# Kernel tuning notes

Hardware: AMD Instinct MI355X
Metric: run time of the kernel (lower is better)

## Reference

```python
import jax, jax.numpy as jnp
import numpy as np

EPS = 1e-7
INF = 1e8
NUM_CLASSES = 80
SOFT_CENTER_RADIUS = 3.0
TOPK = 13
IOU_WEIGHT = 3.0

B, N, G, C = 16, 8400, 100, NUM_CLASSES
IMG = 640.0


def setup_inputs() -> dict:
    key = jax.random.key(0)
    ks = jax.random.split(key, 8)
    # anchor priors: centers in image, stride column (cx, cy, s, s)
    ctr = jax.random.uniform(ks[0], (N, 2)) * IMG
    stride = jnp.full((N, 1), 8.0)
    priors = jnp.concatenate([ctr, stride, stride], axis=-1)
    # predicted boxes: xyxy around random centers
    pc = jax.random.uniform(ks[1], (B, N, 2)) * IMG
    pwh = jax.random.uniform(ks[2], (B, N, 2)) * 64.0 + 8.0
    pred_bboxes = jnp.concatenate([pc - pwh / 2, pc + pwh / 2], axis=-1)
    pred_scores = jax.random.normal(ks[3], (B, N, C))
    # gt boxes: xyxy
    gc = jax.random.uniform(ks[4], (B, G, 2)) * (IMG - 40.0) + 20.0
    gwh = jax.random.uniform(ks[5], (B, G, 2)) * 128.0 + 16.0
    gt_bboxes = jnp.concatenate([gc - gwh / 2, gc + gwh / 2], axis=-1)
    gt_labels = jax.random.randint(ks[6], (B, G, 1), 0, NUM_CLASSES, dtype=jnp.int32)
    pad_bbox_flag = jnp.ones((B, G, 1), dtype=jnp.float32)
    gt_bboxes_area = gwh[..., 0] * gwh[..., 1]
    area_rule = jnp.array([0.0, 32.0, 96.0, 1.0e4], dtype=jnp.float32)
    return {
        'pred_bboxes': pred_bboxes, 'pred_scores': pred_scores, 'priors': priors,
        'gt_labels': gt_labels, 'gt_bboxes': gt_bboxes, 'pad_bbox_flag': pad_bbox_flag,
        'gt_bboxes_area': gt_bboxes_area, 'area_rule': area_rule,
    }


def _giou(b1, b2):
    # b1, b2 broadcastable [..., 4] xyxy -> GIoU [...]
    lt = jnp.maximum(b1[..., :2], b2[..., :2])
    rb = jnp.minimum(b1[..., 2:], b2[..., 2:])
    wh = jnp.clip(rb - lt, 0.0)
    overlap = wh[..., 0] * wh[..., 1]
    a1 = (b1[..., 2] - b1[..., 0]) * (b1[..., 3] - b1[..., 1])
    a2 = (b2[..., 2] - b2[..., 0]) * (b2[..., 3] - b2[..., 1])
    union = jnp.maximum(a1 + a2 - overlap, EPS)
    iou = overlap / union
    elt = jnp.minimum(b1[..., :2], b2[..., :2])
    erb = jnp.maximum(b1[..., 2:], b2[..., 2:])
    ewh = jnp.clip(erb - elt, 0.0)
    enclose = jnp.maximum(ewh[..., 0] * ewh[..., 1], EPS)
    return iou - (enclose - union) / enclose


def _forward(pred_bboxes, pred_scores, priors, gt_labels, gt_bboxes, pad_bbox_flag,
             gt_bboxes_area, area_rule):
    b, n, _ = pred_bboxes.shape
    g = gt_bboxes.shape[1]
    pts = priors[:, :2]                      # (N,2)
    # point-in-box test -> (B,N,G)
    lt = pts[None, :, None, :] - gt_bboxes[:, None, :, :2]
    rb = gt_bboxes[:, None, :, 2:] - pts[None, :, None, :]
    deltas = jnp.concatenate([lt, rb], axis=-1)          # (B,N,G,4)
    is_in = (jnp.min(deltas, axis=-1) > 0).astype(pred_bboxes.dtype)
    is_in = is_in * pad_bbox_flag[:, None, :, 0]
    # soft center prior
    gt_ctr = (gt_bboxes[..., :2] + gt_bboxes[..., 2:]) / 2.0
    strides = priors[:, 2]
    dist = jnp.sqrt(((pts[None, :, None, :] - gt_ctr[:, None, :, :]) ** 2).sum(-1))
    dist = dist / strides[None, :, None] * is_in
    soft_center_prior = jnp.power(10.0, dist - SOFT_CENTER_RADIUS) * is_in
    # pairwise GIoU (B,N,G)
    giou = _giou(pred_bboxes[:, :, None, :], gt_bboxes[:, None, :, :])
    pairwise_ious = jnp.abs(giou * is_in)
    iou_cost = -jnp.log(pairwise_ious + EPS) * IOU_WEIGHT
    # per-gt-class logit gather: (B,N,G)
    labels = gt_labels[..., 0].astype(jnp.int32)         # (B,G)
    idx = jnp.broadcast_to(labels[:, None, :], (b, n, g))
    logits = jnp.take_along_axis(pred_scores, idx, axis=2)
    sig = jax.nn.sigmoid(logits)
    scale = pairwise_ious - sig
    # stable BCE-with-logits against soft target pairwise_ious
    bce = jnp.maximum(logits, 0.0) - logits * pairwise_ious + jnp.log1p(jnp.exp(-jnp.abs(logits)))
    cls_cost = bce * jnp.exp(jnp.abs(scale) - 1.0) * jnp.abs(scale)
    cost = cls_cost + iou_cost + soft_center_prior
    in_mask = is_in > 0
    cost = jnp.where(in_mask, cost, INF)
    # dynamic-k matching
    k = min(TOPK, n)
    topk_ious = jax.lax.top_k(jnp.transpose(pairwise_ious, (0, 2, 1)), k)[0]  # (B,G,k)
    dyn_k = jnp.clip(topk_ious.sum(-1).astype(jnp.int32), 1, None)            # (B,G)
    ranks = jnp.argsort(jnp.argsort(cost, axis=1), axis=1)                    # (B,N,G)
    valid_gt = pad_bbox_flag[..., 0] > 0                                      # (B,G)
    matching = (ranks < dyn_k[:, None, :]) & valid_gt[:, None, :]             # (B,N,G)
    # resolve anchors matched to >1 gt: keep min-cost gt
    multi = matching.sum(-1) > 1                                              # (B,N)
    onehot_min = jax.nn.one_hot(jnp.argmin(cost, axis=-1), g, dtype=jnp.bool_)
    matching = jnp.where(multi[..., None], onehot_min, matching)
    fg_mask = matching.sum(-1) > 0                                            # (B,N)
    mf = matching.astype(pairwise_ious.dtype)
    matched_ious = (mf * pairwise_ious).sum(-1)                               # (B,N)
    matched_gt = jnp.argmax(mf, axis=-1)                                      # (B,N)
    # dense assignments
    assigned_labels = jnp.where(fg_mask, jnp.take_along_axis(labels, matched_gt, axis=1), NUM_CLASSES)
    gidx = jnp.broadcast_to(matched_gt[..., None], (b, n, 4))
    assigned_bboxes = jnp.where(fg_mask[..., None], jnp.take_along_axis(gt_bboxes, gidx, axis=1), 0.0)
    assign_metrics = jnp.where(fg_mask, matched_ious, 0.0)
    onehot = jax.nn.one_hot(assigned_labels, NUM_CLASSES + 1, dtype=pred_scores.dtype)[..., :NUM_CLASSES]
    assigned_scores = onehot * jnp.where(fg_mask, matched_ious, 1.0)[..., None]
    # per-class positive counts and dynamic class weights
    assigned_labels_num = (onehot * fg_mask[..., None].astype(onehot.dtype)).sum((0, 1))
    maxc = assigned_labels_num.max()
    dynamic_gt_class_weight = jnp.where(assigned_labels_num > 0,
                                        maxc / jnp.maximum(assigned_labels_num, 1.0), 1.0)
    assigned_labels_weights = jnp.where(fg_mask[..., None],
                                        dynamic_gt_class_weight[None, None, :],
                                        jnp.ones((), pred_scores.dtype))
    # gt area distribution (len(area_rule)-1, B, G)
    r2 = area_rule ** 2
    ga = gt_bboxes_area[None]
    area_dist = (ga >= r2[:-1, None, None]) & (ga < r2[1:, None, None]) & valid_gt[None]
    return (assigned_labels.astype(jnp.int32), assigned_labels_weights, assigned_bboxes,
            assigned_scores, assign_metrics, fg_mask, assigned_labels_num,
            dynamic_gt_class_weight, area_dist)


def reference(pred_bboxes, pred_scores, priors, gt_labels, gt_bboxes, pad_bbox_flag,
              gt_bboxes_area, area_rule):
    return _forward(pred_bboxes, pred_scores, priors, gt_labels, gt_bboxes,
                    pad_bbox_flag, gt_bboxes_area, area_rule)
```

## Files before the change

kernel.cpp:

```cpp
#include <hip/hip_runtime.h>

typedef unsigned long long u64;

#define BB 16
#define NN 8400
#define GG 100
#define CC 80
#define KTOP 13
#define EPSF 1e-7f
#define INFC 1e8f
#define MAXIN 1024

static constexpr size_t kO_LAB  = 0;
static constexpr size_t kO_W    = (size_t)BB * NN;
static constexpr size_t kO_BB   = kO_W + (size_t)BB * NN * CC;
static constexpr size_t kO_SC   = kO_BB + (size_t)BB * NN * 4;
static constexpr size_t kO_MET  = kO_SC + (size_t)BB * NN * CC;
static constexpr size_t kO_FG   = kO_MET + (size_t)BB * NN;
static constexpr size_t kO_NUM  = kO_FG + (size_t)BB * NN;
static constexpr size_t kO_DYNW = kO_NUM + CC;
static constexpr size_t kO_AREA = kO_DYNW + CC;

__device__ __forceinline__ unsigned f2u(float x) {
    unsigned b = __float_as_uint(x);
    return (b & 0x80000000u) ? ~b : (b | 0x80000000u);
}
__device__ __forceinline__ float u2f(unsigned e) {
    return __uint_as_float((e & 0x80000000u) ? (e & 0x7fffffffu) : ~e);
}

__device__ __forceinline__ void pair_cost_iou_inside(
    float px, float py, float st,
    float p0, float p1, float p2, float p3,
    float g0, float g1, float g2, float g3,
    float lg, float flag,
    float& cost, float& piou)
{
    float gcx = (g0 + g2) * 0.5f, gcy = (g1 + g3) * 0.5f;
    float dx = px - gcx, dy = py - gcy;
    float dist = sqrtf(dx * dx + dy * dy) / st * flag;
    float scp = exp2f((dist - 3.0f) * 3.32192809488736f) * flag;
    float ix1 = fmaxf(p0, g0), iy1 = fmaxf(p1, g1);
    float ix2 = fminf(p2, g2), iy2 = fminf(p3, g3);
    float ow = fmaxf(ix2 - ix1, 0.0f), oh = fmaxf(iy2 - iy1, 0.0f);
    float ov = ow * oh;
    float a1 = (p2 - p0) * (p3 - p1);
    float a2 = (g2 - g0) * (g3 - g1);
    float uni = fmaxf(a1 + a2 - ov, EPSF);
    float iou = ov / uni;
    float ex1 = fminf(p0, g0), ey1 = fminf(p1, g1);
    float ex2 = fmaxf(p2, g2), ey2 = fmaxf(p3, g3);
    float ew = fmaxf(ex2 - ex1, 0.0f), eh = fmaxf(ey2 - ey1, 0.0f);
    float enc = fmaxf(ew * eh, EPSF);
    float giou = iou - (enc - uni) / enc;
    piou = fabsf(giou * flag);
    float iou_cost = -__logf(piou + EPSF) * 3.0f;
    float sig = 1.0f / (1.0f + __expf(-lg));
    float sc = piou - sig;
    float asc = fabsf(sc);
    float bce = fmaxf(lg, 0.0f) - lg * piou + log1pf(__expf(-fabsf(lg)));
    float cls = bce * __expf(asc - 1.0f) * asc;
    cost = cls + iou_cost + scp;
}

__device__ __forceinline__ void pair_cost_iou(
    float px, float py, float st,
    float p0, float p1, float p2, float p3,
    float g0, float g1, float g2, float g3,
    float lg, float flag,
    float& cost, float& piou)
{
    float l = px - g0, t = py - g1, r = g2 - px, d = g3 - py;
    float mn = fminf(fminf(l, t), fminf(r, d));
    float is_in = (mn > 0.0f) ? flag : 0.0f;
    float gcx = (g0 + g2) * 0.5f, gcy = (g1 + g3) * 0.5f;
    float dx = px - gcx, dy = py - gcy;
    float dist = sqrtf(dx * dx + dy * dy) / st * is_in;
    float scp = exp2f((dist - 3.0f) * 3.32192809488736f) * is_in;
    float ix1 = fmaxf(p0, g0), iy1 = fmaxf(p1, g1);
    float ix2 = fminf(p2, g2), iy2 = fminf(p3, g3);
    float ow = fmaxf(ix2 - ix1, 0.0f), oh = fmaxf(iy2 - iy1, 0.0f);
    float ov = ow * oh;
    float a1 = (p2 - p0) * (p3 - p1);
    float a2 = (g2 - g0) * (g3 - g1);
    float uni = fmaxf(a1 + a2 - ov, EPSF);
    float iou = ov / uni;
    float ex1 = fminf(p0, g0), ey1 = fminf(p1, g1);
    float ex2 = fmaxf(p2, g2), ey2 = fmaxf(p3, g3);
    float ew = fmaxf(ex2 - ex1, 0.0f), eh = fmaxf(ey2 - ey1, 0.0f);
    float enc = fmaxf(ew * eh, EPSF);
    float giou = iou - (enc - uni) / enc;
    piou = fabsf(giou * is_in);
    float iou_cost = -__logf(piou + EPSF) * 3.0f;
    float sig = 1.0f / (1.0f + __expf(-lg));
    float sc = piou - sig;
    float asc = fabsf(sc);
    float bce = fmaxf(lg, 0.0f) - lg * piou + log1pf(__expf(-fabsf(lg)));
    float cls = bce * __expf(asc - 1.0f) * asc;
    float cc = cls + iou_cost + scp;
    cost = (is_in > 0.0f) ? cc : INFC;
}

__global__ __launch_bounds__(256) void k1_match(
    const float* __restrict__ pred_bboxes,
    const float* __restrict__ pred_scores,
    const float* __restrict__ priors,
    const int*   __restrict__ gt_labels,
    const float* __restrict__ gt_bboxes,
    const float* __restrict__ pad_flag,
    int*   __restrict__ match_count,
    int*   __restrict__ match_g,
    float* __restrict__ match_iou)
{
    __shared__ int   s_cnt;
    __shared__ int   s_list[MAXIN];
    __shared__ u64   s_kiou[MAXIN];
    __shared__ u64   s_kcost[MAXIN];
    __shared__ unsigned short s_rc[MAXIN];
    __shared__ float s_top[KTOP];

    int bg = blockIdx.x;
    int b = bg / GG, g = bg - b * GG;
    int tid = threadIdx.x;

    float flag = pad_flag[bg];
    if (flag == 0.0f) return;

    if (tid == 0) s_cnt = 0;
    if (tid < KTOP) s_top[tid] = 0.0f;
    __syncthreads();

    float4 gb = *reinterpret_cast<const float4*>(gt_bboxes + (size_t)bg * 4);

    #pragma unroll 4
    for (int k = 0; k < 32; ++k) {
        int n = tid + (k << 8);
        float4 p = *reinterpret_cast<const float4*>(priors + (size_t)n * 4);
        float mn = fminf(fminf(p.x - gb.x, p.y - gb.y),
                         fminf(gb.z - p.x, gb.w - p.y));
        if (mn > 0.0f) {
            int po = atomicAdd(&s_cnt, 1);
            if (po < MAXIN) s_list[po] = n;
        }
    }
    if (tid < NN - 8192) {
        int n = tid + 8192;
        float4 p = *reinterpret_cast<const float4*>(priors + (size_t)n * 4);
        float mn = fminf(fminf(p.x - gb.x, p.y - gb.y),
                         fminf(gb.z - p.x, gb.w - p.y));
        if (mn > 0.0f) {
            int po = atomicAdd(&s_cnt, 1);
            if (po < MAXIN) s_list[po] = n;
        }
    }
    __syncthreads();
    int M = min(s_cnt, MAXIN);

    if (M == 0) {
        if (tid == 0) {
            int idx = b * NN;
            atomicAdd(&match_count[idx], 1);
            match_g[idx]   = g;
            match_iou[idx] = 0.0f;
        }
        return;
    }

    int lab = gt_labels[bg];

    for (int m = tid; m < M; m += 256) {
        int n = s_list[m];
        float4 pr = *reinterpret_cast<const float4*>(priors + (size_t)n * 4);
        float4 pb = *reinterpret_cast<const float4*>(pred_bboxes + ((size_t)b * NN + n) * 4);
        float lg = pred_scores[((size_t)b * NN + n) * CC + lab];
        float cost, piou;
        pair_cost_iou_inside(pr.x, pr.y, pr.z, pb.x, pb.y, pb.z, pb.w,
                             gb.x, gb.y, gb.z, gb.w, lg, flag, cost, piou);
        s_kiou[m]  = ((u64)f2u(piou) << 32) | (unsigned)n;
        s_kcost[m] = ((u64)f2u(cost) << 32) | (unsigned)n;
    }
    __syncthreads();

    for (int m = tid; m < M; m += 256) {
        u64 ki = s_kiou[m];
        u64 kc = s_kcost[m];
        int riou = 0, rcost = 0;
        #pragma unroll 4
        for (int i = 0; i < M; ++i) {
            riou  += (s_kiou[i]  > ki) ? 1 : 0;
            rcost += (s_kcost[i] < kc) ? 1 : 0;
        }
        if (riou < KTOP) s_top[riou] = u2f((unsigned)(ki >> 32));
        s_rc[m] = (unsigned short)rcost;
    }
    __syncthreads();

    float ksum = 0.0f;
    #pragma unroll
    for (int r = 0; r < KTOP; ++r) ksum += s_top[r];
    int dyn_k = (int)ksum;
    if (dyn_k < 1) dyn_k = 1;

    for (int m = tid; m < M; m += 256) {
        if ((int)s_rc[m] < dyn_k) {
            u64 ki = s_kiou[m];
            int n = (int)(ki & 0xffffffffu);
            int idx = b * NN + n;
            atomicAdd(&match_count[idx], 1);
            match_g[idx]   = g;
            match_iou[idx] = u2f((unsigned)(ki >> 32));
        }
    }
}

__global__ __launch_bounds__(256) void k2_resolve(
    const float* __restrict__ pred_bboxes,
    const float* __restrict__ pred_scores,
    const float* __restrict__ priors,
    const int*   __restrict__ gt_labels,
    const float* __restrict__ gt_bboxes,
    const float* __restrict__ pad_flag,
    const int*   __restrict__ match_count,
    const int*   __restrict__ match_g,
    const float* __restrict__ match_iou,
    int*   __restrict__ r_lab,
    float* __restrict__ r_miou,
    int*   __restrict__ class_num,
    float* __restrict__ out)
{
    int i = blockIdx.x * 256 + threadIdx.x;
    int lane = threadIdx.x & 63;
    int cnt = match_count[i];
    int b = i / NN;

    int lab = CC;
    float miou = 0.0f;
    float4 bbx = make_float4(0.0f, 0.0f, 0.0f, 0.0f);

    if (cnt == 1) {
        int g = match_g[i];
        int gi = b * GG + g;
        miou = match_iou[i];
        lab = gt_labels[gi];
        bbx = *reinterpret_cast<const float4*>(gt_bboxes + (size_t)gi * 4);
    }

    u64 mask = __ballot(cnt > 1);
    while (mask) {
        int src = __builtin_ctzll(mask);
        mask &= mask - 1;
        int ii = (i & ~63) | src;
        int b2 = ii / NN, n2 = ii - b2 * NN;
        float4 pr = *reinterpret_cast<const float4*>(priors + (size_t)n2 * 4);
        float4 pb = *reinterpret_cast<const float4*>(pred_bboxes + (size_t)ii * 4);
        u64 bk = ~0ull; float bp = 0.0f;
        #pragma unroll
        for (int s = 0; s < 2; ++s) {
            int gg = lane + (s << 6);
            if (gg < GG) {
                int gi = b2 * GG + gg;
                float fl = pad_flag[gi];
                float4 gbx = *reinterpret_cast<const float4*>(gt_bboxes + (size_t)gi * 4);
                int lb = gt_labels[gi];
                float lg = pred_scores[(size_t)ii * CC + lb];
                float cost, piou;
                pair_cost_iou(pr.x, pr.y, pr.z, pb.x, pb.y, pb.z, pb.w,
                              gbx.x, gbx.y, gbx.z, gbx.w, lg, fl, cost, piou);
                u64 k = ((u64)f2u(cost) << 32) | (unsigned)gg;
                if (k < bk) { bk = k; bp = piou; }
            }
        }
        #pragma unroll
        for (int off = 1; off < 64; off <<= 1) {
            u64 ok = __shfl_xor(bk, off, 64);
            float op = __shfl_xor(bp, off, 64);
            if (ok < bk) { bk = ok; bp = op; }
        }
        if (lane == src) {
            int gw = (int)(bk & 0xffffffffu);
            int gi = b2 * GG + gw;
            lab = gt_labels[gi];
            miou = bp;
            bbx = *reinterpret_cast<const float4*>(gt_bboxes + (size_t)gi * 4);
        }
    }

    bool fg = cnt > 0;
    if (fg) atomicAdd(&class_num[lab], 1);
    r_lab[i]  = lab;
    r_miou[i] = miou;
    out[kO_LAB + i] = (float)lab;
    out[kO_FG  + i] = fg ? 1.0f : 0.0f;
    out[kO_MET + i] = miou;
    *reinterpret_cast<float4*>(out + kO_BB + (size_t)i * 4) = bbx;
}

#define K4MAIN ((BB * NN * (CC / 4)) / 256)
__global__ __launch_bounds__(256) void k4_fill(
    const int*   __restrict__ r_lab,
    const float* __restrict__ r_miou,
    const int*   __restrict__ class_num,
    const float* __restrict__ gt_area,
    const float* __restrict__ area_rule,
    const float* __restrict__ pad_flag,
    float* __restrict__ out)
{
    __shared__ float s_w[CC];
    int t0 = threadIdx.x;
    if (t0 < 64) {
        int n0 = class_num[t0];
        int n1 = (t0 < CC - 64) ? class_num[t0 + 64] : 0;
        int m = max(n0, n1);
        #pragma unroll
        for (int off = 32; off > 0; off >>= 1) m = max(m, __shfl_down(m, off, 64));
        m = __shfl(m, 0, 64);
        float fm = (float)m;
        s_w[t0] = (n0 > 0) ? fm / fmaxf((float)n0, 1.0f) : 1.0f;
        if (t0 < CC - 64)
            s_w[t0 + 64] = (n1 > 0) ? fm / fmaxf((float)n1, 1.0f) : 1.0f;
    }
    __syncthreads();

    unsigned bid = blockIdx.x;
    if (bid < K4MAIN) {
        unsigned t = bid * 256u + threadIdx.x;
        unsigned i = t / 20u;
        unsigned cq = (t - i * 20u) * 4u;
        int lab = r_lab[i];
        float miou = r_miou[i];
        bool fg = lab < CC;
        unsigned ulab = (unsigned)lab;
        float4 sc, wv;
        sc.x = (ulab == cq + 0u) ? miou : 0.0f;
        sc.y = (ulab == cq + 1u) ? miou : 0.0f;
        sc.z = (ulab == cq + 2u) ? miou : 0.0f;
        sc.w = (ulab == cq + 3u) ? miou : 0.0f;
        wv.x = fg ? s_w[cq + 0u] : 1.0f;
        wv.y = fg ? s_w[cq + 1u] : 1.0f;
        wv.z = fg ? s_w[cq + 2u] : 1.0f;
        wv.w = fg ? s_w[cq + 3u] : 1.0f;
        size_t base = (size_t)i * CC + cq;
        *reinterpret_cast<float4*>(out + kO_SC + base) = sc;
        *reinterpret_cast<float4*>(out + kO_W  + base) = wv;
    } else {
        int idx = (int)(bid - K4MAIN) * 256 + threadIdx.x;
        if (idx < 3 * BB * GG) {
            int z = idx / (BB * GG);
            int rem = idx - z * (BB * GG);
            float ga = gt_area[rem];
            float lo = area_rule[z] * area_rule[z];
            float hi = area_rule[z + 1] * area_rule[z + 1];
            bool v = (ga >= lo) && (ga < hi) && (pad_flag[rem] > 0.0f);
            out[kO_AREA + idx] = v ? 1.0f : 0.0f;
        } else if (idx < 3 * BB * GG + CC) {
            int c = idx - 3 * BB * GG;
            out[kO_NUM + c] = (float)class_num[c];
        } else if (idx < 3 * BB * GG + 2 * CC) {
            int c = idx - 3 * BB * GG - CC;
            out[kO_DYNW + c] = s_w[c];
        }
    }
}

extern "C" void kernel_launch(void* const* d_in, const int* in_sizes, int n_in,
                              void* d_out, int out_size, void* d_ws, size_t ws_size,
                              hipStream_t stream)
{
    const float* pred_bboxes = (const float*)d_in[0];
    const float* pred_scores = (const float*)d_in[1];
    const float* priors      = (const float*)d_in[2];
    const int*   gt_labels   = (const int*)d_in[3];
    const float* gt_bboxes   = (const float*)d_in[4];
    const float* pad_flag    = (const float*)d_in[5];
    const float* gt_area     = (const float*)d_in[6];
    const float* area_rule   = (const float*)d_in[7];
    float* out = (float*)d_out;

    char* w = (char*)d_ws;
    int*   match_count = (int*)w;   w += (size_t)BB * NN * 4;
    int*   class_num   = (int*)w;   w += (size_t)CC * 4;
    int*   match_g     = (int*)w;   w += (size_t)BB * NN * 4;
    float* match_iou   = (float*)w; w += (size_t)BB * NN * 4;
    int*   r_lab       = (int*)w;   w += (size_t)BB * NN * 4;
    float* r_miou      = (float*)w; w += (size_t)BB * NN * 4;

    hipMemsetAsync(d_ws, 0, (size_t)(BB * NN + CC) * 4, stream);

    k1_match<<<BB * GG, 256, 0, stream>>>(
        pred_bboxes, pred_scores, priors, gt_labels, gt_bboxes, pad_flag,
        match_count, match_g, match_iou);

    k2_resolve<<<BB * NN / 256, 256, 0, stream>>>(
        pred_bboxes, pred_scores, priors, gt_labels, gt_bboxes, pad_flag,
        match_count, match_g, match_iou, r_lab, r_miou, class_num, out);

    k4_fill<<<K4MAIN + (3 * BB * GG + 2 * CC + 255) / 256, 256, 0, stream>>>(
        r_lab, r_miou, class_num, gt_area, area_rule, pad_flag, out);
}
```

Baseline: 223.3 us.

## Bin priors into a spatial grid to prune the per-GT inside-box scan

A new single-block kernel sorts the priors into a 16x16 grid of 40-pixel cells. It records each cell's start offset and stores a binned copy of each prior with its original index packed into the w field. The matching kernel then scans only the cells that overlap each GT box, not all 8400 priors, which cuts the global loads and compares per block. The fill kernel also switches its large one-hot score and weight outputs to nontemporal stores. The cost is an extra launch and a serial single-block prepass.

```diff
diff --git a/kernel.cpp b/kernel.cpp
--- a/kernel.cpp
+++ b/kernel.cpp
@@ -1,6 +1,7 @@
 #include <hip/hip_runtime.h>
 
 typedef unsigned long long u64;
+typedef float f32x4 __attribute__((ext_vector_type(4)));
 
 #define BB 16
 #define NN 8400
@@ -10,6 +11,7 @@
 #define EPSF 1e-7f
 #define INFC 1e8f
 #define MAXIN 1024
+#define NBIN 16
 
 static constexpr size_t kO_LAB  = 0;
 static constexpr size_t kO_W    = (size_t)BB * NN;
@@ -101,13 +103,58 @@
     cost = (is_in > 0.0f) ? cc : INFC;
 }
 
+__global__ __launch_bounds__(1024) void k0_bin(
+    const float* __restrict__ priors,
+    int*    __restrict__ bin_start,
+    float4* __restrict__ binned)
+{
+    __shared__ int s_cnt[NBIN * NBIN];
+    __shared__ int s_scan[NBIN * NBIN];
+    __shared__ int s_cur[NBIN * NBIN];
+    int tid = threadIdx.x;
+    if (tid < NBIN * NBIN) s_cnt[tid] = 0;
+    __syncthreads();
+    for (int n = tid; n < NN; n += 1024) {
+        float px = priors[(size_t)n * 4 + 0];
+        float py = priors[(size_t)n * 4 + 1];
+        int bx = min(NBIN - 1, (int)(px * 0.025f));
+        int by = min(NBIN - 1, (int)(py * 0.025f));
+        atomicAdd(&s_cnt[by * NBIN + bx], 1);
+    }
+    __syncthreads();
+    if (tid < NBIN * NBIN) s_scan[tid] = s_cnt[tid];
+    __syncthreads();
+    for (int off = 1; off < NBIN * NBIN; off <<= 1) {
+        int v = 0;
+        if (tid < NBIN * NBIN && tid >= off) v = s_scan[tid - off];
+        __syncthreads();
+        if (tid < NBIN * NBIN) s_scan[tid] += v;
+        __syncthreads();
+    }
+    if (tid < NBIN * NBIN) {
+        int ex = s_scan[tid] - s_cnt[tid];
+        s_cur[tid] = ex;
+        bin_start[tid] = ex;
+    }
+    if (tid == 0) bin_start[NBIN * NBIN] = NN;
+    __syncthreads();
+    for (int n = tid; n < NN; n += 1024) {
+        float4 p = *reinterpret_cast<const float4*>(priors + (size_t)n * 4);
+        int bx = min(NBIN - 1, (int)(p.x * 0.025f));
+        int by = min(NBIN - 1, (int)(p.y * 0.025f));
+        int pos = atomicAdd(&s_cur[by * NBIN + bx], 1);
+        binned[pos] = make_float4(p.x, p.y, p.z, __uint_as_float((unsigned)n));
+    }
+}
+
 __global__ __launch_bounds__(256) void k1_match(
-    const float* __restrict__ pred_bboxes,
-    const float* __restrict__ pred_scores,
-    const float* __restrict__ priors,
-    const int*   __restrict__ gt_labels,
-    const float* __restrict__ gt_bboxes,
-    const float* __restrict__ pad_flag,
+    const float*  __restrict__ pred_bboxes,
+    const float*  __restrict__ pred_scores,
+    const int*    __restrict__ gt_labels,
+    const float*  __restrict__ gt_bboxes,
+    const float*  __restrict__ pad_flag,
+    const int*    __restrict__ bin_start,
+    const float4* __restrict__ binned,
     int*   __restrict__ match_count,
     int*   __restrict__ match_g,
     float* __restrict__ match_iou)
@@ -132,25 +179,21 @@
 
     float4 gb = *reinterpret_cast<const float4*>(gt_bboxes + (size_t)bg * 4);
 
-    #pragma unroll 4
-    for (int k = 0; k < 32; ++k) {
-        int n = tid + (k << 8);
-        float4 p = *reinterpret_cast<const float4*>(priors + (size_t)n * 4);
-        float mn = fminf(fminf(p.x - gb.x, p.y - gb.y),
-                         fminf(gb.z - p.x, gb.w - p.y));
-        if (mn > 0.0f) {
-            int po = atomicAdd(&s_cnt, 1);
-            if (po < MAXIN) s_list[po] = n;
-        }
-    }
-    if (tid < NN - 8192) {
-        int n = tid + 8192;
-        float4 p = *reinterpret_cast<const float4*>(priors + (size_t)n * 4);
-        float mn = fminf(fminf(p.x - gb.x, p.y - gb.y),
-                         fminf(gb.z - p.x, gb.w - p.y));
-        if (mn > 0.0f) {
-            int po = atomicAdd(&s_cnt, 1);
-            if (po < MAXIN) s_list[po] = n;
+    int bx0 = min(NBIN - 1, max(0, (int)floorf(gb.x * 0.025f)));
+    int bx1 = min(NBIN - 1, max(0, (int)floorf(gb.z * 0.025f)));
+    int by0 = min(NBIN - 1, max(0, (int)floorf(gb.y * 0.025f)));
+    int by1 = min(NBIN - 1, max(0, (int)floorf(gb.w * 0.025f)));
+    for (int by = by0; by <= by1; ++by) {
+        int r0 = bin_start[by * NBIN + bx0];
+        int r1 = bin_start[by * NBIN + bx1 + 1];
+        for (int m = r0 + tid; m < r1; m += 256) {
+            float4 q = binned[m];
+            float mn = fminf(fminf(q.x - gb.x, q.y - gb.y),
+                             fminf(gb.z - q.x, gb.w - q.y));
+            if (mn > 0.0f) {
+                int po = atomicAdd(&s_cnt, 1);
+                if (po < MAXIN) s_list[po] = m;
+            }
         }
     }
     __syncthreads();
@@ -169,12 +212,12 @@
     int lab = gt_labels[bg];
 
     for (int m = tid; m < M; m += 256) {
-        int n = s_list[m];
-        float4 pr = *reinterpret_cast<const float4*>(priors + (size_t)n * 4);
+        float4 q = binned[s_list[m]];
+        int n = (int)__float_as_uint(q.w);
         float4 pb = *reinterpret_cast<const float4*>(pred_bboxes + ((size_t)b * NN + n) * 4);
         float lg = pred_scores[((size_t)b * NN + n) * CC + lab];
         float cost, piou;
-        pair_cost_iou_inside(pr.x, pr.y, pr.z, pb.x, pb.y, pb.z, pb.w,
+        pair_cost_iou_inside(q.x, q.y, q.z, pb.x, pb.y, pb.z, pb.w,
                              gb.x, gb.y, gb.z, gb.w, lg, flag, cost, piou);
         s_kiou[m]  = ((u64)f2u(piou) << 32) | (unsigned)n;
         s_kcost[m] = ((u64)f2u(cost) << 32) | (unsigned)n;
@@ -330,7 +373,7 @@
         float miou = r_miou[i];
         bool fg = lab < CC;
         unsigned ulab = (unsigned)lab;
-        float4 sc, wv;
+        f32x4 sc, wv;
         sc.x = (ulab == cq + 0u) ? miou : 0.0f;
         sc.y = (ulab == cq + 1u) ? miou : 0.0f;
         sc.z = (ulab == cq + 2u) ? miou : 0.0f;
@@ -340,8 +383,8 @@
         wv.z = fg ? s_w[cq + 2u] : 1.0f;
         wv.w = fg ? s_w[cq + 3u] : 1.0f;
         size_t base = (size_t)i * CC + cq;
-        *reinterpret_cast<float4*>(out + kO_SC + base) = sc;
-        *reinterpret_cast<float4*>(out + kO_W  + base) = wv;
+        __builtin_nontemporal_store(sc, reinterpret_cast<f32x4*>(out + kO_SC + base));
+        __builtin_nontemporal_store(wv, reinterpret_cast<f32x4*>(out + kO_W  + base));
     } else {
         int idx = (int)(bid - K4MAIN) * 256 + threadIdx.x;
         if (idx < 3 * BB * GG) {
@@ -377,18 +420,22 @@
     float* out = (float*)d_out;
 
     char* w = (char*)d_ws;
-    int*   match_count = (int*)w;   w += (size_t)BB * NN * 4;
-    int*   class_num   = (int*)w;   w += (size_t)CC * 4;
-    int*   match_g     = (int*)w;   w += (size_t)BB * NN * 4;
-    float* match_iou   = (float*)w; w += (size_t)BB * NN * 4;
-    int*   r_lab       = (int*)w;   w += (size_t)BB * NN * 4;
-    float* r_miou      = (float*)w; w += (size_t)BB * NN * 4;
-
-    hipMemsetAsync(d_ws, 0, (size_t)(BB * NN + CC) * 4, stream);
+    int*   match_count = (int*)w;    w += (size_t)BB * NN * 4;
+    int*   class_num   = (int*)w;    w += (size_t)CC * 4;
+    int*   match_g     = (int*)w;    w += (size_t)BB * NN * 4;
+    float* match_iou   = (float*)w;  w += (size_t)BB * NN * 4;
+    int*   r_lab       = (int*)w;    w += (size_t)BB * NN * 4;
+    float* r_miou      = (float*)w;  w += (size_t)BB * NN * 4;
+    int*   bin_start   = (int*)w;    w += 1040;
+    float4* binned     = (float4*)w; w += (size_t)NN * 16;
+
+    (void)hipMemsetAsync(d_ws, 0, (size_t)(BB * NN + CC) * 4, stream);
+
+    k0_bin<<<1, 1024, 0, stream>>>(priors, bin_start, binned);
 
     k1_match<<<BB * GG, 256, 0, stream>>>(
-        pred_bboxes, pred_scores, priors, gt_labels, gt_bboxes, pad_flag,
-        match_count, match_g, match_iou);
+        pred_bboxes, pred_scores, gt_labels, gt_bboxes, pad_flag,
+        bin_start, binned, match_count, match_g, match_iou);
 
     k2_resolve<<<BB * NN / 256, 256, 0, stream>>>(
         pred_bboxes, pred_scores, priors, gt_labels, gt_bboxes, pad_flag,
```

After: 225.8 us. No clear change (+1.1%).
